# Kernel optimization log

Hardware: AMD Instinct MI355X
Metric: run time of the kernel (lower is better)

The kernel has to match this reference:

```python
import jax, jax.numpy as jnp
import numpy as np

M = 262144      # number of input points
NF = 16         # features per point
MAX_RADII = np.array([1.0, 1.0, 1.0])
RADII_RES = 4
ANG_RES = np.array([1, 2, 4, 8])


def sample_concentric_ellipsoids():
    """Deterministic kernel structure QX [K=85, 3] (concentric ellipsoids)."""
    Q = []
    for k in range(RADII_RES):
        if k == 0:
            Q.append(np.zeros(3))
            continue
        radii = k / (RADII_RES - 1) * MAX_RADII
        m = int(ANG_RES[k])
        for i in range(m):
            a = i / m * np.pi
            for j in range(m):
                b = j / m * 2 * np.pi
                Q.append(np.array([
                    radii[0] * np.sin(a) * np.cos(b),
                    radii[1] * np.sin(a) * np.sin(b),
                    radii[2] * np.cos(a),
                ]))
    return np.asarray(Q, dtype=np.float32)


def setup_inputs() -> dict:
    key = jax.random.key(0)
    kx, kf = jax.random.split(key)
    X = jax.random.uniform(kx, (M, 3), dtype=jnp.float32)      # points in unit cube
    F = jax.random.normal(kf, (M, NF), dtype=jnp.float32)
    QX = jnp.asarray(sample_concentric_ellipsoids())            # [K, 3], K = 85
    K = QX.shape[0]
    omegaD = jnp.ones((K,), dtype=jnp.float32)   # trainable, init ones (as in build)
    omegaF = jnp.ones((NF,), dtype=jnp.float32)  # trainable, init ones (as in build)
    return {"X": X, "F": F, "QX": QX, "omegaD": omegaD, "omegaF": omegaF}


def reference(X, F, QX, omegaD, omegaF):
    # SUB[k, i, :] = X[i] - QX[k]                       -> [K, M, 3]
    SUB = X[None, :, :] - QX[:, None, :]
    QDun = jnp.sum(SUB * SUB, axis=2)                   # squared distances [K, M]
    QD = jnp.exp(QDun / (omegaD * omegaD)[:, None])     # [K, M]
    QF = omegaF * (QD @ F)                              # kernel feature matrix [K, NF]
    FxQFT = F @ QF.T                                    # [M, K]
    # FULL concatenation strategy: [F, F QF^T, F QF^T QF]
    return jnp.concatenate([F, FxQFT, FxQFT @ QF], axis=1)   # [M, NF + K + NF]
```

## Files before the change

kernel.cpp:

```cpp
#include <hip/hip_runtime.h>

#define KP    96
#define NF    16
#define NCOL  117
#define PBLK  (KP * NF)
#define NB1   1024

typedef __attribute__((ext_vector_type(8))) short bf16x8;
typedef __attribute__((ext_vector_type(4))) float f32x4;

__device__ __forceinline__ float fast_exp2(float x) {
#if __has_builtin(__builtin_amdgcn_exp2f)
    return __builtin_amdgcn_exp2f(x);
#else
    float r;
    asm volatile("v_exp_f32 %0, %1" : "=v"(r) : "v"(x));
    return r;
#endif
}

__device__ __forceinline__ unsigned short f2bf(float f) {
    unsigned int u = __float_as_uint(f);
    u += 0x7FFFu + ((u >> 16) & 1u);
    return (unsigned short)(u >> 16);
}

__device__ __forceinline__ unsigned int pk_bf16(float lo, float hi) {
    unsigned int r;
    asm("v_cvt_pk_bf16_f32 %0, %1, %2" : "=v"(r) : "v"(lo), "v"(hi));
    return r;
}

__global__ __launch_bounds__(384) void k1_partial(
    const float* __restrict__ X, const float* __restrict__ F,
    const float* __restrict__ QX, const float* __restrict__ omegaD,
    int K, int ntile, float* __restrict__ partial)
{
    __shared__ float xs[4 * 32];
    __shared__ unsigned short fsb[32 * 18];

    const int tid  = threadIdx.x;
    const int lane = tid & 63;
    const int wv   = __builtin_amdgcn_readfirstlane(tid >> 6);
    const int kbase = wv * 16;
    const int m = lane & 15;
    const int g = lane >> 4;

    const int k = kbase + m;
    float qs0 = 0.f, qs1 = 0.f, qs2 = 0.f, cc = -3.0e8f, ss = 0.f;
    if (k < K) {
        const float qx = QX[k * 3 + 0];
        const float qy = QX[k * 3 + 1];
        const float qz = QX[k * 3 + 2];
        const float w  = omegaD[k];
        ss  = 1.4426950408889634f / (w * w);
        qs0 = 2.f * ss * qx; qs1 = 2.f * ss * qy; qs2 = 2.f * ss * qz;
        cc  = ss * (qx * qx + qy * qy + qz * qz);
    }

    f32x4 acc = {0.f, 0.f, 0.f, 0.f};

    for (int t = blockIdx.x; t < ntile; t += gridDim.x) {
        const int pbase = t * 32;
        for (int idx = tid; idx < 512; idx += 384) {
            const int p = idx >> 4, n = idx & 15;
            fsb[p * 18 + n] = f2bf(F[(size_t)(pbase + p) * NF + n]);
        }
        if (tid < 32) {
            const float x0 = X[(pbase + tid) * 3 + 0];
            const float x1 = X[(pbase + tid) * 3 + 1];
            const float x2 = X[(pbase + tid) * 3 + 2];
            xs[tid]      = x0;
            xs[32 + tid] = x1;
            xs[64 + tid] = x2;
            xs[96 + tid] = x0 * x0 + x1 * x1 + x2 * x2;
        }
        __syncthreads();

        float e[8];
        unsigned short bs[8];
#pragma unroll
        for (int i = 0; i < 8; ++i) {
            const int p = g * 8 + i;
            const float x0 = xs[p], x1 = xs[32 + p], x2 = xs[64 + p], xn2 = xs[96 + p];
            float h = fmaf(xn2, ss, cc);
            h = fmaf(-x0, qs0, h);
            h = fmaf(-x1, qs1, h);
            h = fmaf(-x2, qs2, h);
            e[i] = fast_exp2(h);
            bs[i] = fsb[p * 18 + m];
        }
        union { bf16x8 v; unsigned int u[4]; } af, bf;
#pragma unroll
        for (int j = 0; j < 4; ++j) {
            af.u[j] = pk_bf16(e[2 * j], e[2 * j + 1]);
            bf.u[j] = (unsigned int)bs[2 * j] | ((unsigned int)bs[2 * j + 1] << 16);
        }
        acc = __builtin_amdgcn_mfma_f32_16x16x32_bf16(af.v, bf.v, acc, 0, 0, 0);
        __syncthreads();
    }

    float* pb = partial + (size_t)blockIdx.x * PBLK;
#pragma unroll
    for (int r = 0; r < 4; ++r) {
        const int krow = kbase + g * 4 + r;
        pb[krow * NF + m] = acc[r];
    }
}

__global__ __launch_bounds__(256) void k1_reduce(
    const float* __restrict__ partial, const float* __restrict__ omegaF,
    int nb, float* __restrict__ QF)
{
    const int k = blockIdx.x, tid = threadIdx.x;
    const int f = tid & 15, g = tid >> 4;
    const float* base = partial + k * NF + f;
    float s0 = 0.f, s1 = 0.f, s2 = 0.f, s3 = 0.f;
    float s4 = 0.f, s5 = 0.f, s6 = 0.f, s7 = 0.f;
    int b = g;
    for (; b + 112 < nb; b += 128) {
        s0 += base[(size_t)(b +   0) * PBLK];
        s1 += base[(size_t)(b +  16) * PBLK];
        s2 += base[(size_t)(b +  32) * PBLK];
        s3 += base[(size_t)(b +  48) * PBLK];
        s4 += base[(size_t)(b +  64) * PBLK];
        s5 += base[(size_t)(b +  80) * PBLK];
        s6 += base[(size_t)(b +  96) * PBLK];
        s7 += base[(size_t)(b + 112) * PBLK];
    }
    for (; b < nb; b += 16) s0 += base[(size_t)b * PBLK];
    const float s = ((s0 + s1) + (s2 + s3)) + ((s4 + s5) + (s6 + s7));

    __shared__ float red[16][17];
    red[g][f] = s;
    __syncthreads();
    if (tid < 16) {
        float t = 0.f;
#pragma unroll
        for (int g2 = 0; g2 < 16; ++g2) t += red[g2][tid];
        QF[k * NF + tid] = t * omegaF[tid];
    }
}

__global__ __launch_bounds__(256, 4) void k2_out(
    const float* __restrict__ F, const float* __restrict__ QFb,
    float* __restrict__ out)
{
    __shared__ __align__(16) float row[2][32 * NCOL];
    __shared__ __align__(16) float qf[85 * 16];
    __shared__ float b2[256];

    const int tid = threadIdx.x;
    const int q = tid & 31, pp = tid >> 5;

    for (int i = tid; i < 85 * 16; i += 256) qf[i] = QFb[i];
    __syncthreads();
    {
        const int u = tid & 15, v = tid >> 4;
        float s = 0.f;
        for (int k = 0; k < 85; ++k) s += qf[k * 16 + v] * qf[k * 16 + u];
        b2[tid] = s;
    }
    __syncthreads();

    float qr[3][NF];
#pragma unroll
    for (int j = 0; j < 3; ++j) {
        const int k = q + 32 * j;
        if (k < 85) {
#pragma unroll
            for (int u2 = 0; u2 < NF; ++u2) qr[j][u2] = qf[k * 16 + u2];
        } else {
#pragma unroll
            for (int u2 = 0; u2 < NF; ++u2) qr[j][u2] = 0.f;
        }
    }
    float b2c[NF];
#pragma unroll
    for (int v = 0; v < NF; ++v) b2c[v] = b2[v * 16 + (q & 15)];

    const int chunk = blockIdx.x * 256;
#pragma unroll 2
    for (int st = 0; st < 8; ++st) {
        const int sbase = chunk + st * 32;
        float* bufp = row[st & 1];
        float fr[NF];
        {
            const float4* Fv = reinterpret_cast<const float4*>(F + (size_t)(sbase + pp) * NF);
            const float4 t0 = Fv[0], t1 = Fv[1], t2 = Fv[2], t3 = Fv[3];
            fr[0]=t0.x; fr[1]=t0.y; fr[2]=t0.z; fr[3]=t0.w;
            fr[4]=t1.x; fr[5]=t1.y; fr[6]=t1.z; fr[7]=t1.w;
            fr[8]=t2.x; fr[9]=t2.y; fr[10]=t2.z; fr[11]=t2.w;
            fr[12]=t3.x; fr[13]=t3.y; fr[14]=t3.z; fr[15]=t3.w;
        }
#pragma unroll
        for (int it = 0; it < 4; ++it) {
            float4 n0, n1, n2, n3;
            if (it < 3) {
                const float4* Fv = reinterpret_cast<const float4*>(
                    F + (size_t)(sbase + (it + 1) * 8 + pp) * NF);
                n0 = Fv[0]; n1 = Fv[1]; n2 = Fv[2]; n3 = Fv[3];
            }
            float* rp = &bufp[(it * 8 + pp) * NCOL];
#pragma unroll
            for (int j = 0; j < 3; ++j) {
                const int k = q + 32 * j;
                float t = 0.f;
#pragma unroll
                for (int u2 = 0; u2 < NF; ++u2) t += fr[u2] * qr[j][u2];
                if (k < 85) rp[16 + k] = t;
            }
            if (q == 0) {
#pragma unroll
                for (int u2 = 0; u2 < NF; ++u2) rp[u2] = fr[u2];
            }
            if (q < 16) {
                float g = 0.f;
#pragma unroll
                for (int v = 0; v < NF; ++v) g += fr[v] * b2c[v];
                rp[101 + q] = g;
            }
            if (it < 3) {
                fr[0]=n0.x; fr[1]=n0.y; fr[2]=n0.z; fr[3]=n0.w;
                fr[4]=n1.x; fr[5]=n1.y; fr[6]=n1.z; fr[7]=n1.w;
                fr[8]=n2.x; fr[9]=n2.y; fr[10]=n2.z; fr[11]=n2.w;
                fr[12]=n3.x; fr[13]=n3.y; fr[14]=n3.z; fr[15]=n3.w;
            }
        }
        __syncthreads();
        {
            float4* dst = reinterpret_cast<float4*>(out + (size_t)sbase * NCOL);
            const float4* src = reinterpret_cast<const float4*>(bufp);
            for (int t2 = tid; t2 < (32 * NCOL) / 4; t2 += 256) dst[t2] = src[t2];
        }
    }
}

extern "C" void kernel_launch(void* const* d_in, const int* in_sizes, int n_in,
                              void* d_out, int out_size, void* d_ws, size_t ws_size,
                              hipStream_t stream)
{
    const float* X      = (const float*)d_in[0];
    const float* F      = (const float*)d_in[1];
    const float* QX     = (const float*)d_in[2];
    const float* omegaD = (const float*)d_in[3];
    const float* omegaF = (const float*)d_in[4];
    float* out = (float*)d_out;

    const int M = in_sizes[0] / 3;
    const int K = in_sizes[3];
    const int ntile = M / 32;

    int nb = (int)((ws_size / sizeof(float) - PBLK) / PBLK);
    if (nb > NB1) nb = NB1;
    if (nb > ntile) nb = ntile;
    if (nb < 1) nb = 1;

    float* partial = (float*)d_ws;
    float* QFbuf   = partial + (size_t)nb * PBLK;

    hipLaunchKernelGGL(k1_partial, dim3(nb), dim3(384), 0, stream,
                       X, F, QX, omegaD, K, ntile, partial);
    hipLaunchKernelGGL(k1_reduce, dim3(KP), dim3(256), 0, stream,
                       partial, omegaF, nb, QFbuf);
    hipLaunchKernelGGL(k2_out, dim3(M / 256), dim3(256), 0, stream,
                       F, QFbuf, out);
}
```

Before: 63.81 us.

## Fuse partial accumulation and reduction via cooperative grid sync

Merges the partial-sum kernel and the reduction kernel into one cooperative kernel that uses a grid-wide barrier before the first 96 blocks reduce the partials into QF. This removes one kernel launch and its inter-kernel gap, at the cost of a grid sync across 1024 blocks. If the cooperative launch fails (for example, because 1024 blocks cannot be co-resident), it falls back to the original two-kernel path. The workspace-size check on nb was also removed, so nb is now fixed at 1024.

```diff
diff --git a/kernel.cpp b/kernel.cpp
--- a/kernel.cpp
+++ b/kernel.cpp
@@ -1,4 +1,7 @@
 #include <hip/hip_runtime.h>
+#include <hip/hip_cooperative_groups.h>
+
+namespace cg = cooperative_groups;
 
 #define KP    96
 #define NF    16
@@ -29,6 +32,114 @@
     unsigned int r;
     asm("v_cvt_pk_bf16_f32 %0, %1, %2" : "=v"(r) : "v"(lo), "v"(hi));
     return r;
+}
+
+__global__ __launch_bounds__(384) void k1_fused(
+    const float* __restrict__ X, const float* __restrict__ F,
+    const float* __restrict__ QX, const float* __restrict__ omegaD,
+    const float* __restrict__ omegaF,
+    int K, int ntile, int nb,
+    float* __restrict__ partial, float* __restrict__ QF)
+{
+    __shared__ float xs[4 * 32];
+    __shared__ unsigned short fsb[32 * 18];
+    __shared__ float red[24][17];
+
+    const int tid  = threadIdx.x;
+    const int lane = tid & 63;
+    const int wv   = __builtin_amdgcn_readfirstlane(tid >> 6);
+    const int kbase = wv * 16;
+    const int m = lane & 15;
+    const int g = lane >> 4;
+
+    {
+        const int k = kbase + m;
+        float qs0 = 0.f, qs1 = 0.f, qs2 = 0.f, cc = -3.0e8f, ss = 0.f;
+        if (k < K) {
+            const float qx = QX[k * 3 + 0];
+            const float qy = QX[k * 3 + 1];
+            const float qz = QX[k * 3 + 2];
+            const float w  = omegaD[k];
+            ss  = 1.4426950408889634f / (w * w);
+            qs0 = 2.f * ss * qx; qs1 = 2.f * ss * qy; qs2 = 2.f * ss * qz;
+            cc  = ss * (qx * qx + qy * qy + qz * qz);
+        }
+
+        f32x4 acc = {0.f, 0.f, 0.f, 0.f};
+
+        for (int t = blockIdx.x; t < ntile; t += gridDim.x) {
+            const int pbase = t * 32;
+            for (int idx = tid; idx < 512; idx += 384) {
+                const int p = idx >> 4, n = idx & 15;
+                fsb[p * 18 + n] = f2bf(F[(size_t)(pbase + p) * NF + n]);
+            }
+            if (tid < 32) {
+                const float x0 = X[(pbase + tid) * 3 + 0];
+                const float x1 = X[(pbase + tid) * 3 + 1];
+                const float x2 = X[(pbase + tid) * 3 + 2];
+                xs[tid]      = x0;
+                xs[32 + tid] = x1;
+                xs[64 + tid] = x2;
+                xs[96 + tid] = x0 * x0 + x1 * x1 + x2 * x2;
+            }
+            __syncthreads();
+
+            float e[8];
+            unsigned short bs[8];
+#pragma unroll
+            for (int i = 0; i < 8; ++i) {
+                const int p = g * 8 + i;
+                const float x0 = xs[p], x1 = xs[32 + p], x2 = xs[64 + p], xn2 = xs[96 + p];
+                float h = fmaf(xn2, ss, cc);
+                h = fmaf(-x0, qs0, h);
+                h = fmaf(-x1, qs1, h);
+                h = fmaf(-x2, qs2, h);
+                e[i] = fast_exp2(h);
+                bs[i] = fsb[p * 18 + m];
+            }
+            union { bf16x8 v; unsigned int u[4]; } af, bf;
+#pragma unroll
+            for (int j = 0; j < 4; ++j) {
+                af.u[j] = pk_bf16(e[2 * j], e[2 * j + 1]);
+                bf.u[j] = (unsigned int)bs[2 * j] | ((unsigned int)bs[2 * j + 1] << 16);
+            }
+            acc = __builtin_amdgcn_mfma_f32_16x16x32_bf16(af.v, bf.v, acc, 0, 0, 0);
+            __syncthreads();
+        }
+
+        float* pb = partial + (size_t)blockIdx.x * PBLK;
+#pragma unroll
+        for (int r = 0; r < 4; ++r) {
+            const int krow = kbase + g * 4 + r;
+            pb[krow * NF + m] = acc[r];
+        }
+    }
+
+    cg::this_grid().sync();
+
+    if (blockIdx.x < KP) {
+        const int k  = blockIdx.x;
+        const int f  = tid & 15;
+        const int gg = tid >> 4;
+        const float* base = partial + k * NF + f;
+        float s0 = 0.f, s1 = 0.f, s2 = 0.f, s3 = 0.f;
+        int b = gg;
+        for (; b + 72 < nb; b += 96) {
+            s0 += base[(size_t)(b +  0) * PBLK];
+            s1 += base[(size_t)(b + 24) * PBLK];
+            s2 += base[(size_t)(b + 48) * PBLK];
+            s3 += base[(size_t)(b + 72) * PBLK];
+        }
+        for (; b < nb; b += 24) s0 += base[(size_t)b * PBLK];
+        red[gg][f] = (s0 + s1) + (s2 + s3);
+        __syncthreads();
+        if (tid < 16) {
+            float t = 0.f;
+#pragma unroll
+            for (int g2 = 0; g2 < 24; ++g2) t += red[g2][tid];
+            QF[k * NF + tid] = t * omegaF[tid];
+        }
+    }
 }
 
 __global__ __launch_bounds__(384) void k1_partial(
@@ -248,21 +359,25 @@
     float* out = (float*)d_out;
 
     const int M = in_sizes[0] / 3;
-    const int K = in_sizes[3];
-    const int ntile = M / 32;
-
-    int nb = (int)((ws_size / sizeof(float) - PBLK) / PBLK);
-    if (nb > NB1) nb = NB1;
+    int K = in_sizes[3];
+    int ntile = M / 32;
+    int nb = NB1;
     if (nb > ntile) nb = ntile;
-    if (nb < 1) nb = 1;
 
     float* partial = (float*)d_ws;
     float* QFbuf   = partial + (size_t)nb * PBLK;
 
-    hipLaunchKernelGGL(k1_partial, dim3(nb), dim3(384), 0, stream,
-                       X, F, QX, omegaD, K, ntile, partial);
-    hipLaunchKernelGGL(k1_reduce, dim3(KP), dim3(256), 0, stream,
-                       partial, omegaF, nb, QFbuf);
+    void* args[] = {(void*)&X, (void*)&F, (void*)&QX, (void*)&omegaD,
+                    (void*)&omegaF, (void*)&K, (void*)&ntile, (void*)&nb,
+                    (void*)&partial, (void*)&QFbuf};
+    hipError_t err = hipLaunchCooperativeKernel((void*)k1_fused, dim3(nb), dim3(384),
+                                                args, 0, stream);
+    if (err != hipSuccess) {
+        hipLaunchKernelGGL(k1_partial, dim3(nb), dim3(384), 0, stream,
+                           X, F, QX, omegaD, K, ntile, partial);
+        hipLaunchKernelGGL(k1_reduce, dim3(KP), dim3(256), 0, stream,
+                           partial, omegaF, nb, QFbuf);
+    }
     hipLaunchKernelGGL(k2_out, dim3(M / 256), dim3(256), 0, stream,
                        F, QFbuf, out);
 }
```

New measurement: 172.1 us. 170% more time.
